# Optimization experiments

Measured on AMD Instinct MI355X. Metric: run time of the kernel, lower is better.

Reference implementation:

```python
import jax, jax.numpy as jnp
import numpy as np

N_QUBITS = 8
DIM = 2 ** N_QUBITS  # 256


def _apply_1q(state, U, q):
    """Apply a single-qubit gate U on wire q. state: (B, 256) complex64.
    U: (2,2) shared gate or (B,2,2) per-sample gate."""
    B = state.shape[0]
    s = state.reshape(B, 2 ** q, 2, 2 ** (N_QUBITS - 1 - q))
    if U.ndim == 2:
        s = jnp.einsum('ij,bajc->baic', U, s)
    else:
        s = jnp.einsum('bij,bajc->baic', U, s)
    return s.reshape(B, DIM)


def _apply_cnot(state, c, t):
    """CNOT with control wire c, target wire t (pure permutation of amplitudes)."""
    B = state.shape[0]
    a, b = (c, t) if c < t else (t, c)
    s = state.reshape(B, 2 ** a, 2, 2 ** (b - a - 1), 2, 2 ** (N_QUBITS - 1 - b))
    if c < t:
        s0 = s[:, :, 0]                       # control=0: unchanged
        s1 = jnp.flip(s[:, :, 1], axis=3)     # control=1: flip target axis
        s = jnp.stack([s0, s1], axis=2)
    else:
        s0 = s[:, :, :, :, 0]
        s1 = jnp.flip(s[:, :, :, :, 1], axis=2)
        s = jnp.stack([s0, s1], axis=4)
    return s.reshape(B, DIM)


def _rx_batch(theta):
    """Batched RX(theta): (B,) -> (B,2,2) complex64."""
    c = jnp.cos(theta / 2).astype(jnp.complex64)
    s = (-1j * jnp.sin(theta / 2)).astype(jnp.complex64)
    return jnp.stack([jnp.stack([c, s], -1), jnp.stack([s, c], -1)], -2)


def _rot(phi, theta, omega):
    """PennyLane Rot(phi,theta,omega) = RZ(omega) RY(theta) RZ(phi) as a 2x2 matrix."""
    c = jnp.cos(theta / 2)
    s = jnp.sin(theta / 2)
    m00 = jnp.exp(-0.5j * (phi + omega)) * c
    m01 = -jnp.exp(0.5j * (phi - omega)) * s
    m10 = jnp.exp(-0.5j * (phi - omega)) * s
    m11 = jnp.exp(0.5j * (phi + omega)) * c
    return jnp.stack([jnp.stack([m00, m01]), jnp.stack([m10, m11])]).astype(jnp.complex64)


def _circuit(x, weights):
    """AngleEmbedding (RX) + StronglyEntanglingLayers, return <Z_i> per wire: (B,8)."""
    B = x.shape[0]
    state = jnp.zeros((B, DIM), jnp.complex64).at[:, 0].set(1.0)
    # AngleEmbedding: RX(x[:, q]) on wire q
    for q in range(N_QUBITS):
        state = _apply_1q(state, _rx_batch(x[:, q]), q)
    n_layers = weights.shape[0]
    for l in range(n_layers):
        for q in range(N_QUBITS):
            state = _apply_1q(state, _rot(weights[l, q, 0], weights[l, q, 1], weights[l, q, 2]), q)
        r = (l % (N_QUBITS - 1)) + 1  # PennyLane default ranges
        for q in range(N_QUBITS):
            state = _apply_cnot(state, q, (q + r) % N_QUBITS)
    probs = state.real ** 2 + state.imag ** 2  # (B, 256)
    bits = (jnp.arange(DIM)[:, None] >> jnp.arange(N_QUBITS - 1, -1, -1)[None, :]) & 1
    signs = (1.0 - 2.0 * bits).astype(probs.dtype)  # (256, 8); wire 0 = MSB
    return probs @ signs  # (B, 8) expectation values of PauliZ


def setup_inputs() -> dict:
    key = jax.random.key(0)
    k1, k2, k3 = jax.random.split(key, 3)
    B = 32768
    x = jax.random.uniform(k1, (B, N_QUBITS), dtype=jnp.float32)
    weights = jax.random.uniform(k2, (2, N_QUBITS, 3), dtype=jnp.float32, maxval=2.0 * np.pi)
    fc_w = jax.random.normal(k3, (1, N_QUBITS), dtype=jnp.float32) / np.sqrt(N_QUBITS)
    fc_b = jnp.zeros((1,), jnp.float32)
    return {"x": x, "weights": weights, "fc_w": fc_w, "fc_b": fc_b}


def reference(x, weights, fc_w, fc_b):
    z = _circuit(x, weights)                 # (B, 8)
    return jax.nn.sigmoid(z @ fc_w.T + fc_b)  # (B, 1)
```

## Files before the change

kernel.cpp:

```cpp
#include <hip/hip_runtime.h>
#include <hip/hip_fp16.h>
#include <math.h>

#define NQ 8

__host__ __device__ constexpr int cnot_step(int i, int c, int t) {
    return ((i >> (7 - c)) & 1) ? (i ^ (1 << (7 - t))) : i;
}
__host__ __device__ constexpr int sigma_fwd(int i, int r) {
    for (int q = 0; q < 8; ++q) i = cnot_step(i, q, (q + r) & 7);
    return i;
}
__host__ __device__ constexpr int sigma_inv(int i, int r) {
    for (int q = 7; q >= 0; --q) i = cnot_step(i, q, (q + r) & 7);
    return i;
}
__host__ __device__ constexpr int pairmask(int q) { return sigma_inv(1 << (7 - q), 1); }
__host__ __device__ constexpr int rolemask(int q) {
    int m = 0;
    for (int j = 0; j < 8; ++j)
        if ((sigma_fwd(1 << j, 1) >> (7 - q)) & 1) m |= 1 << j;
    return m;
}
__host__ __device__ constexpr int colmask2(int b) {
    return sigma_fwd(sigma_fwd(1 << b, 1), 2);
}

__host__ __device__ constexpr int amp_index(int slot, int k, int hl) {
    return (slot << 7) | (((k >> 2) & 1) << 6) | (((hl >> 3) & 1) << 5)
         | (((hl >> 2) & 1) << 4) | (((hl >> 1) & 1) << 3) | ((hl & 1) << 2)
         | (((k >> 1) & 1) << 1) | (k & 1);
}
__host__ __device__ constexpr int mask_slot(int M) { return (M >> 7) & 1; }
__host__ __device__ constexpr int mask_k(int M) {
    return (((M >> 6) & 1) << 2) | (((M >> 1) & 1) << 1) | (M & 1);
}
__host__ __device__ constexpr int mask_l(int M) { return (M >> 2) & 15; }

__device__ __forceinline__ __half2 bc_h2(uint32_t u) { return __builtin_bit_cast(__half2, u); }
__device__ __forceinline__ uint32_t bc_u32(__half2 h) { return __builtin_bit_cast(uint32_t, h); }
__device__ __forceinline__ uint32_t rot16(uint32_t u) { return (u >> 16) | (u << 16); }

template<int XM>
__device__ __forceinline__ uint32_t swzu(uint32_t v) {
    return (uint32_t)__builtin_amdgcn_ds_swizzle((int)v, (XM << 10) | 0x1F);
}
template<int XM>
__device__ __forceinline__ float swzf(float v) {
    return __builtin_bit_cast(float, (uint32_t)__builtin_amdgcn_ds_swizzle(
        (int)__builtin_bit_cast(uint32_t, v), (XM << 10) | 0x1F));
}

__device__ __forceinline__ void cmul(float& zr, float& zi,
                                     float xr, float xi, float yr, float yi) {
    const float tr = xr * yr - xi * yi;
    const float ti = xr * yi + xi * yr;
    zr = tr; zi = ti;
}

__device__ __forceinline__ void colq(const float* __restrict__ g, float xh,
                                     float& ar, float& ai, float& br, float& bi) {
    float sn, cs; __sincosf(xh, &sn, &cs);
    ar = cs * g[0] + sn * g[3];
    ai = cs * g[1] - sn * g[2];
    br = cs * g[4] + sn * g[7];
    bi = cs * g[5] - sn * g[6];
}

template<int Q>
__device__ __forceinline__ void gateQ(__half2 re[8], __half2 im[8], int hl,
                                      const uint32_t* __restrict__ cw)
{
    constexpr int M  = pairmask(Q);
    constexpr int RM = rolemask(Q);
    constexpr int mk = mask_k(M);
    constexpr int ml = mask_l(M);
    constexpr int ms = mask_slot(M);
    constexpr int rk = mask_k(RM);
    constexpr int rl = mask_l(RM);

    const uint4    c4  = *(const uint4*)(cw + Q * 8);
    const uint32_t WDn = cw[Q * 8 + 4];

    const uint32_t pm = (uint32_t)(__popc(hl & rl) & 1) * 0x80008000u;
    const uint32_t Bp = c4.y ^ pm, Bn = Bp ^ 0x80008000u;
    const uint32_t Cp = c4.z ^ pm, Cn = Cp ^ 0x80008000u;
    const __half2  Aw = bc_h2(c4.x);
    const __half2  Dw = bc_h2(c4.w);
    const __half2  Dn = bc_h2(WDn);

    uint32_t pre[8], pim[8];
#pragma unroll
    for (int k = 0; k < 8; ++k) {
        uint32_t vr = bc_u32(re[k ^ mk]);
        uint32_t vi = bc_u32(im[k ^ mk]);
        if constexpr (ms) { vr = rot16(vr); vi = rot16(vi); }
        if constexpr (ml) { vr = swzu<ml>(vr); vi = swzu<ml>(vi); }
        pre[k] = vr; pim[k] = vi;
    }
#pragma unroll
    for (int k = 0; k < 8; ++k) {
        const bool par = (__popc(k & rk) & 1) != 0;
        const __half2 B1 = bc_h2(par ? Bn : Bp);
        const __half2 B2 = bc_h2(par ? Bp : Bn);
        const __half2 Cc = bc_h2(par ? Cn : Cp);
        __half2 nr = __hmul2(Aw, re[k]);
        nr = __hfma2(B1, im[k], nr);
        nr = __hfma2(Cc, bc_h2(pre[k]), nr);
        nr = __hfma2(Dw, bc_h2(pim[k]), nr);
        __half2 ni = __hmul2(Aw, im[k]);
        ni = __hfma2(B2, re[k], ni);
        ni = __hfma2(Cc, bc_h2(pim[k]), ni);
        ni = __hfma2(Dn, bc_h2(pre[k]), ni);
        re[k] = nr; im[k] = ni;
    }
}

__global__ __launch_bounds__(256) void vqe_fused(
    const float* __restrict__ x,
    const float* __restrict__ weights,
    const float* __restrict__ fc_w,
    const float* __restrict__ fc_b,
    float* __restrict__ out, int B)
{
    __shared__ __align__(16) float    g0[64];
    __shared__ __align__(16) uint32_t cw[64];
    __shared__ __align__(16) float    wtab[16 * 20];

    const int t = threadIdx.x;

    if (t < 8) {
        const float* w3 = weights + t * 3;
        float s, c;   __sincosf(w3[1] * 0.5f, &s, &c);
        float sa, ca; __sincosf(0.5f * (w3[0] + w3[2]), &sa, &ca);
        float sb, cb; __sincosf(0.5f * (w3[0] - w3[2]), &sb, &cb);
        float* g = g0 + t * 8;
        g[0] = c * ca;  g[1] = -c * sa;
        g[2] = -s * cb; g[3] = -s * sb;
        g[4] = s * cb;  g[5] = -s * sb;
        g[6] = c * ca;  g[7] = c * sa;
    } else if (t < 16) {
        const int q = t - 8;
        const float* w3 = weights + (NQ + q) * 3;
        float s, c;   __sincosf(w3[1] * 0.5f, &s, &c);
        float sa, ca; __sincosf(0.5f * (w3[0] + w3[2]), &sa, &ca);
        float sb, cb; __sincosf(0.5f * (w3[0] - w3[2]), &sb, &cb);
        const float A = c * ca, Bc = c * sa, C = s * cb, D = s * sb;
        const float s1 = (rolemask(q) & 0x80) ? -1.f : 1.f;
        uint32_t* cq = cw + q * 8;
        cq[0] = bc_u32(__floats2half2_rn(A, A));
        cq[1] = bc_u32(__floats2half2_rn(Bc, s1 * Bc));
        cq[2] = bc_u32(__floats2half2_rn(-C, -s1 * C));
        cq[3] = bc_u32(__floats2half2_rn(D, D));
        cq[4] = bc_u32(__floats2half2_rn(-D, -D));
        cq[5] = 0; cq[6] = 0; cq[7] = 0;
    }
    {
        const int whl = t >> 4, wk = (t >> 1) & 7, wslot = t & 1;
        const int s = amp_index(wslot, wk, whl);
        int j = 0;
#pragma unroll
        for (int b = 0; b < 8; ++b)
            if ((s >> b) & 1) j ^= colmask2(b);
        float w = 0.f;
#pragma unroll
        for (int q = 0; q < 8; ++q)
            w += ((j >> (7 - q)) & 1) ? -fc_w[q] : fc_w[q];
        wtab[whl * 20 + wk * 2 + wslot] = w;
    }
    __syncthreads();

    const int lane = t & 63;
    const int hl   = lane & 15;
    const int samp = (int)((blockIdx.x * blockDim.x + t) >> 6) * 4 + (lane >> 4);
    if (samp >= B) return;

    const float4 x0 = ((const float4*)(x + samp * NQ))[0];
    const float4 x1 = ((const float4*)(x + samp * NQ))[1];
    const float xq[8] = {x0.x, x0.y, x0.z, x0.w, x1.x, x1.y, x1.z, x1.w};

    float cr, ci;
    {
        const float* g = g0 + 2 * 8 + ((hl >> 3) & 1) * 4;
        float sn, cs; __sincosf(xq[2] * 0.5f, &sn, &cs);
        cr = cs * g[0] + sn * g[3];
        ci = cs * g[1] - sn * g[2];
    }
#pragma unroll
    for (int q = 3; q < 6; ++q) {
        const float* g = g0 + q * 8 + ((hl >> (5 - q)) & 1) * 4;
        float sn, cs; __sincosf(xq[q] * 0.5f, &sn, &cs);
        const float yr = cs * g[0] + sn * g[3];
        const float yi = cs * g[1] - sn * g[2];
        cmul(cr, ci, cr, ci, yr, yi);
    }

    float a1r, a1i, b1r, b1i, a6r, a6i, b6r, b6i, a7r, a7i, b7r, b7i, a0r, a0i, b0r, b0i;
    colq(g0 + 1 * 8, xq[1] * 0.5f, a1r, a1i, b1r, b1i);
    colq(g0 + 6 * 8, xq[6] * 0.5f, a6r, a6i, b6r, b6i);
    colq(g0 + 7 * 8, xq[7] * 0.5f, a7r, a7i, b7r, b7i);
    colq(g0 + 0 * 8, xq[0] * 0.5f, a0r, a0i, b0r, b0i);

    float u1r[2], u1i[2];
    cmul(u1r[0], u1i[0], cr, ci, a1r, a1i);
    cmul(u1r[1], u1i[1], cr, ci, b1r, b1i);
    float u2r[4], u2i[4];
    cmul(u2r[0], u2i[0], u1r[0], u1i[0], a6r, a6i);
    cmul(u2r[1], u2i[1], u1r[0], u1i[0], b6r, b6i);
    cmul(u2r[2], u2i[2], u1r[1], u1i[1], a6r, a6i);
    cmul(u2r[3], u2i[3], u1r[1], u1i[1], b6r, b6i);
    float u3r[8], u3i[8];
#pragma unroll
    for (int k = 0; k < 8; ++k) {
        const float vr = (k & 1) ? b7r : a7r;
        const float vi = (k & 1) ? b7i : a7i;
        cmul(u3r[k], u3i[k], u2r[k >> 1], u2i[k >> 1], vr, vi);
    }

    const __half2 Vre  = __floats2half2_rn(a0r, b0r);
    const __half2 Vim  = __floats2half2_rn(a0i, b0i);
    const __half2 Vimn = bc_h2(bc_u32(Vim) ^ 0x80008000u);
    __half2 re[8], im[8];
#pragma unroll
    for (int k = 0; k < 8; ++k) {
        const __half2 Ur = __floats2half2_rn(u3r[k], u3r[k]);
        const __half2 Ui = __floats2half2_rn(u3i[k], u3i[k]);
        re[k] = __hfma2(Ui, Vimn, __hmul2(Ur, Vre));
        im[k] = __hfma2(Ui, Vre,  __hmul2(Ur, Vim));
    }

    gateQ<0>(re, im, hl, cw);
    gateQ<1>(re, im, hl, cw);
    gateQ<2>(re, im, hl, cw);
    gateQ<3>(re, im, hl, cw);
    gateQ<4>(re, im, hl, cw);
    gateQ<5>(re, im, hl, cw);
    gateQ<6>(re, im, hl, cw);
    gateQ<7>(re, im, hl, cw);

    const float* wl = wtab + hl * 20;
    const float4 w0 = *(const float4*)(wl + 0);
    const float4 w1 = *(const float4*)(wl + 4);
    const float4 w2 = *(const float4*)(wl + 8);
    const float4 w3 = *(const float4*)(wl + 12);
    const float wv[16] = {w0.x, w0.y, w0.z, w0.w, w1.x, w1.y, w1.z, w1.w,
                          w2.x, w2.y, w2.z, w2.w, w3.x, w3.y, w3.z, w3.w};

    float acc = 0.f;
#pragma unroll
    for (int k = 0; k < 8; ++k) {
        const float rl_ = __low2float(re[k]),  rh_ = __high2float(re[k]);
        const float il_ = __low2float(im[k]),  ih_ = __high2float(im[k]);
        acc = fmaf(rl_ * rl_ + il_ * il_, wv[k * 2 + 0], acc);
        acc = fmaf(rh_ * rh_ + ih_ * ih_, wv[k * 2 + 1], acc);
    }
    acc += swzf<1>(acc);
    acc += swzf<2>(acc);
    acc += swzf<4>(acc);
    acc += swzf<8>(acc);

    if (hl == 0) {
        const float z = acc + fc_b[0];
        out[samp] = 1.0f / (1.0f + __expf(-z));
    }
}

extern "C" void kernel_launch(void* const* d_in, const int* in_sizes, int n_in,
                              void* d_out, int out_size, void* d_ws, size_t ws_size,
                              hipStream_t stream) {
    const float* x       = (const float*)d_in[0];
    const float* weights = (const float*)d_in[1];
    const float* fc_w    = (const float*)d_in[2];
    const float* fc_b    = (const float*)d_in[3];
    float* out = (float*)d_out;

    const int B = in_sizes[0] / NQ;
    const int waves  = (B + 3) / 4;
    const int blocks = (waves + 3) / 4;

    vqe_fused<<<blocks, 256, 0, stream>>>(x, weights, fc_w, fc_b, out, B);
}
```

Baseline: 20.98 us.

## Precompute per-sample embedding columns in shared memory and use fp16 product-state build

Moves the per-qubit sincos and first-layer gate column computation from every lane (16 lanes per sample recomputed all 8) into one thread per (sample, qubit), stored in shared memory behind an extra barrier. The initial product state is then built with packed half2 complex multiplies instead of fp32, and the final weighted probability reduction uses fp16 weights with fdot2. The gate loop is reordered into pairwise processing, and launch bounds request 8 blocks per CU. This trades redundant transcendental work for an additional sync and more fp16 rounding in state construction.

```diff
diff --git a/kernel.cpp b/kernel.cpp
--- a/kernel.cpp
+++ b/kernel.cpp
@@ -37,8 +37,11 @@
 }
 __host__ __device__ constexpr int mask_l(int M) { return (M >> 2) & 15; }
 
+typedef _Float16 h2v __attribute__((ext_vector_type(2)));
+
 __device__ __forceinline__ __half2 bc_h2(uint32_t u) { return __builtin_bit_cast(__half2, u); }
 __device__ __forceinline__ uint32_t bc_u32(__half2 h) { return __builtin_bit_cast(uint32_t, h); }
+__device__ __forceinline__ h2v bc_hv(__half2 h) { return __builtin_bit_cast(h2v, h); }
 __device__ __forceinline__ uint32_t rot16(uint32_t u) { return (u >> 16) | (u << 16); }
 
 template<int XM>
@@ -58,13 +61,12 @@
     zr = tr; zi = ti;
 }
 
-__device__ __forceinline__ void colq(const float* __restrict__ g, float xh,
-                                     float& ar, float& ai, float& br, float& bi) {
-    float sn, cs; __sincosf(xh, &sn, &cs);
-    ar = cs * g[0] + sn * g[3];
-    ai = cs * g[1] - sn * g[2];
-    br = cs * g[4] + sn * g[7];
-    bi = cs * g[5] - sn * g[6];
+struct H2C { __half2 re, im; };
+__device__ __forceinline__ H2C h2c_mul(H2C x, __half2 yre, __half2 yim, __half2 yimn) {
+    H2C z;
+    z.re = __hfma2(x.im, yimn, __hmul2(x.re, yre));
+    z.im = __hfma2(x.im, yre,  __hmul2(x.re, yim));
+    return z;
 }
 
 template<int Q>
@@ -79,44 +81,61 @@
     constexpr int rk = mask_k(RM);
     constexpr int rl = mask_l(RM);
 
-    const uint4    c4  = *(const uint4*)(cw + Q * 8);
+    const uint4    c4v = *(const uint4*)(cw + Q * 8);
     const uint32_t WDn = cw[Q * 8 + 4];
 
     const uint32_t pm = (uint32_t)(__popc(hl & rl) & 1) * 0x80008000u;
-    const uint32_t Bp = c4.y ^ pm, Bn = Bp ^ 0x80008000u;
-    const uint32_t Cp = c4.z ^ pm, Cn = Cp ^ 0x80008000u;
-    const __half2  Aw = bc_h2(c4.x);
-    const __half2  Dw = bc_h2(c4.w);
+    const uint32_t Bp = c4v.y ^ pm, Bn = Bp ^ 0x80008000u;
+    const uint32_t Cp = c4v.z ^ pm, Cn = Cp ^ 0x80008000u;
+    const __half2  Aw = bc_h2(c4v.x);
+    const __half2  Dw = bc_h2(c4v.w);
     const __half2  Dn = bc_h2(WDn);
 
-    uint32_t pre[8], pim[8];
-#pragma unroll
-    for (int k = 0; k < 8; ++k) {
-        uint32_t vr = bc_u32(re[k ^ mk]);
-        uint32_t vi = bc_u32(im[k ^ mk]);
-        if constexpr (ms) { vr = rot16(vr); vi = rot16(vi); }
-        if constexpr (ml) { vr = swzu<ml>(vr); vi = swzu<ml>(vi); }
-        pre[k] = vr; pim[k] = vi;
-    }
-#pragma unroll
-    for (int k = 0; k < 8; ++k) {
+    auto prep = [](uint32_t v) -> uint32_t {
+        if constexpr (ms) v = rot16(v);
+        if constexpr (ml) v = swzu<ml>(v);
+        return v;
+    };
+    auto upd = [&](int k, uint32_t pr, uint32_t pi) {
         const bool par = (__popc(k & rk) & 1) != 0;
         const __half2 B1 = bc_h2(par ? Bn : Bp);
         const __half2 B2 = bc_h2(par ? Bp : Bn);
         const __half2 Cc = bc_h2(par ? Cn : Cp);
         __half2 nr = __hmul2(Aw, re[k]);
         nr = __hfma2(B1, im[k], nr);
-        nr = __hfma2(Cc, bc_h2(pre[k]), nr);
-        nr = __hfma2(Dw, bc_h2(pim[k]), nr);
+        nr = __hfma2(Cc, bc_h2(pr), nr);
+        nr = __hfma2(Dw, bc_h2(pi), nr);
         __half2 ni = __hmul2(Aw, im[k]);
         ni = __hfma2(B2, re[k], ni);
-        ni = __hfma2(Cc, bc_h2(pim[k]), ni);
-        ni = __hfma2(Dn, bc_h2(pre[k]), ni);
+        ni = __hfma2(Cc, bc_h2(pi), ni);
+        ni = __hfma2(Dn, bc_h2(pr), ni);
         re[k] = nr; im[k] = ni;
-    }
-}
-
-__global__ __launch_bounds__(256) void vqe_fused(
+    };
+
+    if constexpr (mk == 0) {
+#pragma unroll
+        for (int k = 0; k < 8; ++k) {
+            const uint32_t pr = prep(bc_u32(re[k]));
+            const uint32_t pi = prep(bc_u32(im[k]));
+            upd(k, pr, pi);
+        }
+    } else {
+        constexpr int msb = (mk & 4) ? 4 : ((mk & 2) ? 2 : 1);
+#pragma unroll
+        for (int k = 0; k < 8; ++k) {
+            if ((k & msb) != 0) continue;
+            const int k2 = k ^ mk;
+            const uint32_t pr_k  = prep(bc_u32(re[k2]));
+            const uint32_t pi_k  = prep(bc_u32(im[k2]));
+            const uint32_t pr_k2 = prep(bc_u32(re[k]));
+            const uint32_t pi_k2 = prep(bc_u32(im[k]));
+            upd(k,  pr_k,  pi_k);
+            upd(k2, pr_k2, pi_k2);
+        }
+    }
+}
+
+__global__ __launch_bounds__(256, 8) void vqe_fused(
     const float* __restrict__ x,
     const float* __restrict__ weights,
     const float* __restrict__ fc_w,
@@ -125,7 +144,8 @@
 {
     __shared__ __align__(16) float    g0[64];
     __shared__ __align__(16) uint32_t cw[64];
-    __shared__ __align__(16) float    wtab[16 * 20];
+    __shared__ __align__(16) float    cols[16 * 36];
+    __shared__ __align__(16) uint32_t wth2[16 * 12];
 
     const int t = threadIdx.x;
 
@@ -154,79 +174,102 @@
         cq[3] = bc_u32(__floats2half2_rn(D, D));
         cq[4] = bc_u32(__floats2half2_rn(-D, -D));
         cq[5] = 0; cq[6] = 0; cq[7] = 0;
-    }
-    {
-        const int whl = t >> 4, wk = (t >> 1) & 7, wslot = t & 1;
-        const int s = amp_index(wslot, wk, whl);
-        int j = 0;
-#pragma unroll
-        for (int b = 0; b < 8; ++b)
-            if ((s >> b) & 1) j ^= colmask2(b);
-        float w = 0.f;
-#pragma unroll
-        for (int q = 0; q < 8; ++q)
-            w += ((j >> (7 - q)) & 1) ? -fc_w[q] : fc_w[q];
-        wtab[whl * 20 + wk * 2 + wslot] = w;
+    } else if (t >= 128) {
+        const int tt = t - 128;
+        const int whl = tt >> 3, wk = tt & 7;
+        float wsl[2];
+#pragma unroll
+        for (int slot = 0; slot < 2; ++slot) {
+            const int s = amp_index(slot, wk, whl);
+            int j = 0;
+#pragma unroll
+            for (int b = 0; b < 8; ++b)
+                if ((s >> b) & 1) j ^= colmask2(b);
+            float w = 0.f;
+#pragma unroll
+            for (int q = 0; q < 8; ++q)
+                w += ((j >> (7 - q)) & 1) ? -fc_w[q] : fc_w[q];
+            wsl[slot] = w;
+        }
+        wth2[whl * 12 + wk] = bc_u32(__floats2half2_rn(wsl[0], wsl[1]));
+    }
+    __syncthreads();
+
+    if (t < 128) {
+        const int s = t >> 3, q = t & 7;
+        const int sg = blockIdx.x * 16 + s;
+        if (sg < B) {
+            const float xv = x[sg * NQ + q];
+            float sn, cs; __sincosf(xv * 0.5f, &sn, &cs);
+            const float* g = g0 + q * 8;
+            float* c = cols + s * 36 + q * 4;
+            c[0] = cs * g[0] + sn * g[3];
+            c[1] = cs * g[1] - sn * g[2];
+            c[2] = cs * g[4] + sn * g[7];
+            c[3] = cs * g[5] - sn * g[6];
+        }
     }
     __syncthreads();
 
     const int lane = t & 63;
     const int hl   = lane & 15;
-    const int samp = (int)((blockIdx.x * blockDim.x + t) >> 6) * 4 + (lane >> 4);
+    const int sidx = ((t >> 6) << 2) | ((lane >> 4) & 3);
+    const int samp = blockIdx.x * 16 + sidx;
     if (samp >= B) return;
 
-    const float4 x0 = ((const float4*)(x + samp * NQ))[0];
-    const float4 x1 = ((const float4*)(x + samp * NQ))[1];
-    const float xq[8] = {x0.x, x0.y, x0.z, x0.w, x1.x, x1.y, x1.z, x1.w};
-
-    float cr, ci;
+    const float* cb = cols + sidx * 36;
+
+    const float2 e2 = *(const float2*)(cb + 2 * 4 + ((hl >> 3) & 1) * 2);
+    const float2 e3 = *(const float2*)(cb + 3 * 4 + ((hl >> 2) & 1) * 2);
+    const float2 e4 = *(const float2*)(cb + 4 * 4 + ((hl >> 1) & 1) * 2);
+    const float2 e5 = *(const float2*)(cb + 5 * 4 + (hl & 1) * 2);
+    float cr = e2.x, ci = e2.y;
+    cmul(cr, ci, cr, ci, e3.x, e3.y);
+    cmul(cr, ci, cr, ci, e4.x, e4.y);
+    cmul(cr, ci, cr, ci, e5.x, e5.y);
+
+    const float4 c0 = *(const float4*)(cb + 0 * 4);
+    const float4 c1 = *(const float4*)(cb + 1 * 4);
+    const float4 c6 = *(const float4*)(cb + 6 * 4);
+    const float4 c7 = *(const float4*)(cb + 7 * 4);
+
+    float w0r, w0i, w1r, w1i;
+    cmul(w0r, w0i, cr, ci, c0.x, c0.y);
+    cmul(w1r, w1i, cr, ci, c0.z, c0.w);
+    H2C S{__floats2half2_rn(w0r, w1r), __floats2half2_rn(w0i, w1i)};
+
+    const __half2 y7ar = __floats2half2_rn(c7.x, c7.x), y7ai = __floats2half2_rn(c7.y, c7.y);
+    const __half2 y7br = __floats2half2_rn(c7.z, c7.z), y7bi = __floats2half2_rn(c7.w, c7.w);
+    const __half2 y7ain = bc_h2(bc_u32(y7ai) ^ 0x80008000u);
+    const __half2 y7bin = bc_h2(bc_u32(y7bi) ^ 0x80008000u);
+    H2C A0 = h2c_mul(S, y7ar, y7ai, y7ain);
+    H2C A1 = h2c_mul(S, y7br, y7bi, y7bin);
+
+    const __half2 y6ar = __floats2half2_rn(c6.x, c6.x), y6ai = __floats2half2_rn(c6.y, c6.y);
+    const __half2 y6br = __floats2half2_rn(c6.z, c6.z), y6bi = __floats2half2_rn(c6.w, c6.w);
+    const __half2 y6ain = bc_h2(bc_u32(y6ai) ^ 0x80008000u);
+    const __half2 y6bin = bc_h2(bc_u32(y6bi) ^ 0x80008000u);
+    H2C B0 = h2c_mul(A0, y6ar, y6ai, y6ain);
+    H2C B1 = h2c_mul(A1, y6ar, y6ai, y6ain);
+    H2C B2 = h2c_mul(A0, y6br, y6bi, y6bin);
+    H2C B3 = h2c_mul(A1, y6br, y6bi, y6bin);
+
+    const __half2 y1ar = __floats2half2_rn(c1.x, c1.x), y1ai = __floats2half2_rn(c1.y, c1.y);
+    const __half2 y1br = __floats2half2_rn(c1.z, c1.z), y1bi = __floats2half2_rn(c1.w, c1.w);
+    const __half2 y1ain = bc_h2(bc_u32(y1ai) ^ 0x80008000u);
+    const __half2 y1bin = bc_h2(bc_u32(y1bi) ^ 0x80008000u);
+
+    __half2 re[8], im[8];
     {
-        const float* g = g0 + 2 * 8 + ((hl >> 3) & 1) * 4;
-        float sn, cs; __sincosf(xq[2] * 0.5f, &sn, &cs);
-        cr = cs * g[0] + sn * g[3];
-        ci = cs * g[1] - sn * g[2];
-    }
-#pragma unroll
-    for (int q = 3; q < 6; ++q) {
-        const float* g = g0 + q * 8 + ((hl >> (5 - q)) & 1) * 4;
-        float sn, cs; __sincosf(xq[q] * 0.5f, &sn, &cs);
-        const float yr = cs * g[0] + sn * g[3];
-        const float yi = cs * g[1] - sn * g[2];
-        cmul(cr, ci, cr, ci, yr, yi);
-    }
-
-    float a1r, a1i, b1r, b1i, a6r, a6i, b6r, b6i, a7r, a7i, b7r, b7i, a0r, a0i, b0r, b0i;
-    colq(g0 + 1 * 8, xq[1] * 0.5f, a1r, a1i, b1r, b1i);
-    colq(g0 + 6 * 8, xq[6] * 0.5f, a6r, a6i, b6r, b6i);
-    colq(g0 + 7 * 8, xq[7] * 0.5f, a7r, a7i, b7r, b7i);
-    colq(g0 + 0 * 8, xq[0] * 0.5f, a0r, a0i, b0r, b0i);
-
-    float u1r[2], u1i[2];
-    cmul(u1r[0], u1i[0], cr, ci, a1r, a1i);
-    cmul(u1r[1], u1i[1], cr, ci, b1r, b1i);
-    float u2r[4], u2i[4];
-    cmul(u2r[0], u2i[0], u1r[0], u1i[0], a6r, a6i);
-    cmul(u2r[1], u2i[1], u1r[0], u1i[0], b6r, b6i);
-    cmul(u2r[2], u2i[2], u1r[1], u1i[1], a6r, a6i);
-    cmul(u2r[3], u2i[3], u1r[1], u1i[1], b6r, b6i);
-    float u3r[8], u3i[8];
-#pragma unroll
-    for (int k = 0; k < 8; ++k) {
-        const float vr = (k & 1) ? b7r : a7r;
-        const float vi = (k & 1) ? b7i : a7i;
-        cmul(u3r[k], u3i[k], u2r[k >> 1], u2i[k >> 1], vr, vi);
-    }
-
-    const __half2 Vre  = __floats2half2_rn(a0r, b0r);
-    const __half2 Vim  = __floats2half2_rn(a0i, b0i);
-    const __half2 Vimn = bc_h2(bc_u32(Vim) ^ 0x80008000u);
-    __half2 re[8], im[8];
-#pragma unroll
-    for (int k = 0; k < 8; ++k) {
-        const __half2 Ur = __floats2half2_rn(u3r[k], u3r[k]);
-        const __half2 Ui = __floats2half2_rn(u3i[k], u3i[k]);
-        re[k] = __hfma2(Ui, Vimn, __hmul2(Ur, Vre));
-        im[k] = __hfma2(Ui, Vre,  __hmul2(Ur, Vim));
+        H2C z;
+        z = h2c_mul(B0, y1ar, y1ai, y1ain); re[0] = z.re; im[0] = z.im;
+        z = h2c_mul(B1, y1ar, y1ai, y1ain); re[1] = z.re; im[1] = z.im;
+        z = h2c_mul(B2, y1ar, y1ai, y1ain); re[2] = z.re; im[2] = z.im;
+        z = h2c_mul(B3, y1ar, y1ai, y1ain); re[3] = z.re; im[3] = z.im;
+        z = h2c_mul(B0, y1br, y1bi, y1bin); re[4] = z.re; im[4] = z.im;
+        z = h2c_mul(B1, y1br, y1bi, y1bin); re[5] = z.re; im[5] = z.im;
+        z = h2c_mul(B2, y1br, y1bi, y1bin); re[6] = z.re; im[6] = z.im;
+        z = h2c_mul(B3, y1br, y1bi, y1bin); re[7] = z.re; im[7] = z.im;
     }
 
     gateQ<0>(re, im, hl, cw);
@@ -238,21 +281,24 @@
     gateQ<6>(re, im, hl, cw);
     gateQ<7>(re, im, hl, cw);
 
-    const float* wl = wtab + hl * 20;
-    const float4 w0 = *(const float4*)(wl + 0);
-    const float4 w1 = *(const float4*)(wl + 4);
-    const float4 w2 = *(const float4*)(wl + 8);
-    const float4 w3 = *(const float4*)(wl + 12);
-    const float wv[16] = {w0.x, w0.y, w0.z, w0.w, w1.x, w1.y, w1.z, w1.w,
-                          w2.x, w2.y, w2.z, w2.w, w3.x, w3.y, w3.z, w3.w};
+    const uint32_t* wrow = wth2 + hl * 12;
+    const uint4 wa = *(const uint4*)(wrow + 0);
+    const uint4 wb = *(const uint4*)(wrow + 4);
+    const uint32_t wk[8] = {wa.x, wa.y, wa.z, wa.w, wb.x, wb.y, wb.z, wb.w};
 
     float acc = 0.f;
 #pragma unroll
     for (int k = 0; k < 8; ++k) {
-        const float rl_ = __low2float(re[k]),  rh_ = __high2float(re[k]);
-        const float il_ = __low2float(im[k]),  ih_ = __high2float(im[k]);
-        acc = fmaf(rl_ * rl_ + il_ * il_, wv[k * 2 + 0], acc);
-        acc = fmaf(rh_ * rh_ + ih_ * ih_, wv[k * 2 + 1], acc);
+        const __half2 W = bc_h2(wk[k]);
+        const __half2 tr_ = __hmul2(re[k], W);
+        const __half2 ti_ = __hmul2(im[k], W);
+#if defined(__has_builtin) && __has_builtin(__builtin_amdgcn_fdot2)
+        acc = __builtin_amdgcn_fdot2(bc_hv(tr_), bc_hv(re[k]), acc, false);
+        acc = __builtin_amdgcn_fdot2(bc_hv(ti_), bc_hv(im[k]), acc, false);
+#else
+        acc += __low2float(tr_) * __low2float(re[k]) + __high2float(tr_) * __high2float(re[k]);
+        acc += __low2float(ti_) * __low2float(im[k]) + __high2float(ti_) * __high2float(im[k]);
+#endif
     }
     acc += swzf<1>(acc);
     acc += swzf<2>(acc);
@@ -275,8 +321,7 @@
     float* out = (float*)d_out;
 
     const int B = in_sizes[0] / NQ;
-    const int waves  = (B + 3) / 4;
-    const int blocks = (waves + 3) / 4;
+    const int blocks = (B + 15) / 16;
 
     vqe_fused<<<blocks, 256, 0, stream>>>(x, weights, fc_w, fc_b, out, B);
 }
```

After: 18.79 us. -10.5%, faster.
